# Performance work log

Measured on AMD Instinct MI355X. Metric: run time of the kernel, lower is better.

The kernel has to match this reference:

```python
import jax, jax.numpy as jnp
import numpy as np

TEXT_MAP_W, BOX_W, CONF_W = 1.0, 1.0, 1.0
LOG_CLAMP = -100.0  # torch F.binary_cross_entropy clamps log terms at -100


def _bce(p, t):
    logp = jnp.maximum(jnp.log(p), LOG_CLAMP)
    log1mp = jnp.maximum(jnp.log1p(-p), LOG_CLAMP)
    return -(t * logp + (1.0 - t) * log1mp)


def _smooth_l1(pred, tgt):
    d = jnp.abs(pred - tgt)
    return jnp.where(d < 1.0, 0.5 * d * d, d - 0.5)


def setup_inputs() -> dict:
    key = jax.random.key(0)
    ks = jax.random.split(key, 6)
    B, H, W, N = 16, 512, 512, 256
    return {
        "text_map_pred": jax.random.uniform(ks[0], (B, 1, H, W), jnp.float32),
        "text_map_tgt": jax.random.uniform(ks[1], (B, 1, H, W), jnp.float32),
        "confidence_pred": jax.random.uniform(ks[2], (B, 1, H, W), jnp.float32),
        "bbox_pred": jax.random.uniform(ks[3], (B, 4, H, W), jnp.float32),
        "box_conf": jax.random.uniform(ks[4], (B, N), jnp.float32),
        "box_xyxy": jax.random.randint(ks[5], (B, N, 4), 0, W, jnp.int64 if jax.config.read('jax_enable_x64') else jnp.int32),
        "box_mask": jnp.ones((B, N), dtype=bool),
    }


def reference(text_map_pred, text_map_tgt, confidence_pred, bbox_pred,
              box_conf, box_xyxy, box_mask):
    B, _, H, W = text_map_pred.shape
    N = box_conf.shape[1]

    # text map loss: pixelwise BCE, mean over all pixels
    text_map_loss = _bce(text_map_pred, text_map_tgt).mean()

    x1 = box_xyxy[..., 0]; y1 = box_xyxy[..., 1]
    x2 = box_xyxy[..., 2]; y2 = box_xyxy[..., 3]
    cx = (x1 + x2) // 2  # int((x1+x2)/2) for nonneg coords
    cy = (y1 + y2) // 2
    valid = box_mask & (cx >= 0) & (cx < W) & (cy >= 0) & (cy < H)  # [B,N]

    cx_c = jnp.clip(cx, 0, W - 1)
    cy_c = jnp.clip(cy, 0, H - 1)
    bi = jnp.arange(B)[:, None]  # [B,1]

    pred_box = bbox_pred[bi, :, cy_c, cx_c]          # [B,N,4]
    pred_cnf = confidence_pred[bi, 0, cy_c, cx_c]    # [B,N]

    fW = jnp.asarray(W, text_map_pred.dtype)
    fH = jnp.asarray(H, text_map_pred.dtype)
    tgt_box = jnp.stack([x1 / fW, y1 / fH, x2 / fW, y2 / fH], axis=-1)  # [B,N,4]

    box_l1 = _smooth_l1(pred_box, tgt_box).mean(axis=-1)  # per-box mean over 4 coords
    conf_l = _bce(pred_cnf, box_conf)                      # [B,N]

    vf = valid.astype(text_map_pred.dtype)
    total_boxes = vf.sum()
    denom = jnp.maximum(total_boxes, 1.0)
    any_valid = total_boxes > 0
    box_loss = jnp.where(any_valid, (box_l1 * vf).sum() / denom, 0.0)
    confidence_loss = jnp.where(any_valid, (conf_l * vf).sum() / denom, 0.0)

    total_loss = (TEXT_MAP_W * text_map_loss + BOX_W * box_loss
                  + CONF_W * confidence_loss)
    return jnp.stack([total_loss, text_map_loss, box_loss, confidence_loss])
```

## Files before the change

kernel.cpp:

```cpp
#include <hip/hip_runtime.h>

namespace {

constexpr int B = 16, H = 512, W = 512, N = 256;
constexpr int HWc = H * W;
constexpr int NBLK = 2048;
constexpr int NTHR = 256;
constexpr float LOG2_CLAMP = -144.26950408889634f;
constexpr float LN2 = 0.69314718055994531f;

constexpr int WS_L1 = NBLK, WS_CL = NBLK + 16, WS_VF = NBLK + 32;

__device__ __forceinline__ float bce2(float p, float t) {
    float m1 = fmaxf(__log2f(p), LOG2_CLAMP);
    float m2 = fmaxf(__log2f(1.0f - p), LOG2_CLAMP);
    return fmaf(t, m2 - m1, -m2);
}

__device__ __forceinline__ float smooth_l1(float pred, float tgt) {
    float d = fabsf(pred - tgt);
    return d < 1.0f ? 0.5f * d * d : d - 0.5f;
}

__device__ __forceinline__ float block_reduce_sum(float v) {
    __shared__ float smem[8];
    for (int off = 32; off > 0; off >>= 1)
        v += __shfl_down(v, off, 64);
    int lane = threadIdx.x & 63, wid = threadIdx.x >> 6;
    __syncthreads();
    if (lane == 0) smem[wid] = v;
    __syncthreads();
    if (threadIdx.x == 0) {
        float s = 0.0f;
        int nw = (int)(blockDim.x >> 6);
        for (int i = 0; i < nw; ++i) s += smem[i];
        v = s;
    }
    return v;
}

__global__ __launch_bounds__(NTHR) void main_kernel(
        const float4* __restrict__ p4,
        const float4* __restrict__ t4,
        const float*  __restrict__ conf_pred,
        const float*  __restrict__ bbox_pred,
        const float*  __restrict__ box_conf,
        const int*    __restrict__ box_xyxy,
        const int*    __restrict__ box_mask,
        float* __restrict__ ws) {
    const int n4 = B * HWc / 4;
    int idx = blockIdx.x * NTHR + threadIdx.x;
    float acc = 0.0f;
    #pragma unroll 2
    for (int i = idx; i < n4; i += NBLK * NTHR) {
        float4 p = p4[i];
        float4 t = t4[i];
        acc += bce2(p.x, t.x) + bce2(p.y, t.y) + bce2(p.z, t.z) + bce2(p.w, t.w);
    }
    float s = block_reduce_sum(acc);
    if (threadIdx.x == 0) ws[blockIdx.x] = s;

    if (blockIdx.x < B) {
        int b = blockIdx.x, n = threadIdx.x;
        int bi = b * N + n;
        int4 xy = reinterpret_cast<const int4*>(box_xyxy)[bi];
        int cx = (xy.x + xy.z) >> 1;
        int cy = (xy.y + xy.w) >> 1;
        bool valid = (box_mask[bi] != 0) && cx >= 0 && cx < W && cy >= 0 && cy < H;
        int cxc = min(max(cx, 0), W - 1);
        int cyc = min(max(cy, 0), H - 1);

        int base = ((b * 4) * H + cyc) * W + cxc;
        float l1 = 0.25f * (smooth_l1(bbox_pred[base          ], (float)xy.x * (1.0f / W)) +
                            smooth_l1(bbox_pred[base +     HWc], (float)xy.y * (1.0f / H)) +
                            smooth_l1(bbox_pred[base + 2 * HWc], (float)xy.z * (1.0f / W)) +
                            smooth_l1(bbox_pred[base + 3 * HWc], (float)xy.w * (1.0f / H)));
        float cl = bce2(conf_pred[(b * H + cyc) * W + cxc], box_conf[bi]);

        float vf = valid ? 1.0f : 0.0f;
        float s1 = block_reduce_sum(l1 * vf);
        float s2 = block_reduce_sum(cl * vf);
        float s3 = block_reduce_sum(vf);
        if (threadIdx.x == 0) {
            ws[WS_L1 + b] = s1;
            ws[WS_CL + b] = s2;
            ws[WS_VF + b] = s3;
        }
    }
}

__global__ __launch_bounds__(512) void finalize_kernel(
        const float* __restrict__ ws, float* __restrict__ out) {
    float s = 0.0f;
    #pragma unroll
    for (int i = threadIdx.x; i < NBLK; i += 512) s += ws[i];
    float text_sum = block_reduce_sum(s);

    float v1 = threadIdx.x < 16 ? ws[WS_L1 + threadIdx.x] : 0.0f;
    float v2 = threadIdx.x < 16 ? ws[WS_CL + threadIdx.x] : 0.0f;
    float v3 = threadIdx.x < 16 ? ws[WS_VF + threadIdx.x] : 0.0f;
    float s1 = block_reduce_sum(v1);
    float s2 = block_reduce_sum(v2);
    float s3 = block_reduce_sum(v3);

    if (threadIdx.x == 0) {
        float text = text_sum * (LN2 / (float)(B * HWc));
        float denom = fmaxf(s3, 1.0f);
        bool any = s3 > 0.0f;
        float box  = any ? s1 / denom : 0.0f;
        float conf = any ? (s2 * LN2) / denom : 0.0f;
        out[0] = text + box + conf;
        out[1] = text;
        out[2] = box;
        out[3] = conf;
    }
}

}

extern "C" void kernel_launch(void* const* d_in, const int* in_sizes, int n_in,
                              void* d_out, int out_size, void* d_ws, size_t ws_size,
                              hipStream_t stream) {
    const float* text_pred = (const float*)d_in[0];
    const float* text_tgt  = (const float*)d_in[1];
    const float* conf_pred = (const float*)d_in[2];
    const float* bbox_pred = (const float*)d_in[3];
    const float* box_conf  = (const float*)d_in[4];
    const int*   box_xyxy  = (const int*)d_in[5];
    const int*   box_mask  = (const int*)d_in[6];

    float* out = (float*)d_out;
    float* ws  = (float*)d_ws;

    main_kernel<<<NBLK, NTHR, 0, stream>>>(
        (const float4*)text_pred, (const float4*)text_tgt,
        conf_pred, bbox_pred, box_conf, box_xyxy, box_mask, ws);
    finalize_kernel<<<1, 512, 0, stream>>>(ws, out);
}
```

Before: 15.55 us.

## Fuse finalize into main kernel via last-block atomic reduction

Drops the separate finalize launch. Each block atomically adds its partial sums into a small set of global slots, and the last block to finish (found with an atomic counter) reduces the slots and writes the four outputs. The grid is also halved to 1024 blocks, each doing a fixed, fully unrolled 4 iterations. This removes one kernel launch and the workspace round trip, in exchange for atomic contention on 32 slots and a counter that relies on modulo wraparound across calls.

```diff
diff --git a/kernel.cpp b/kernel.cpp
--- a/kernel.cpp
+++ b/kernel.cpp
@@ -4,12 +4,16 @@
 
 constexpr int B = 16, H = 512, W = 512, N = 256;
 constexpr int HWc = H * W;
-constexpr int NBLK = 2048;
+constexpr int NBLK = 1024;
 constexpr int NTHR = 256;
+constexpr int TEXT_SLOTS = 32;
 constexpr float LOG2_CLAMP = -144.26950408889634f;
 constexpr float LN2 = 0.69314718055994531f;
 
-constexpr int WS_L1 = NBLK, WS_CL = NBLK + 16, WS_VF = NBLK + 32;
+__device__ float    g_slot[TEXT_SLOTS + 3 * 16];
+__device__ unsigned g_cnt;
+
+constexpr int SL_L1 = TEXT_SLOTS, SL_CL = TEXT_SLOTS + 16, SL_VF = TEXT_SLOTS + 32;
 
 __device__ __forceinline__ float bce2(float p, float t) {
     float m1 = fmaxf(__log2f(p), LOG2_CLAMP);
@@ -23,23 +27,18 @@
 }
 
 __device__ __forceinline__ float block_reduce_sum(float v) {
-    __shared__ float smem[8];
+    __shared__ float smem[4];
     for (int off = 32; off > 0; off >>= 1)
         v += __shfl_down(v, off, 64);
     int lane = threadIdx.x & 63, wid = threadIdx.x >> 6;
     __syncthreads();
     if (lane == 0) smem[wid] = v;
     __syncthreads();
-    if (threadIdx.x == 0) {
-        float s = 0.0f;
-        int nw = (int)(blockDim.x >> 6);
-        for (int i = 0; i < nw; ++i) s += smem[i];
-        v = s;
-    }
+    if (threadIdx.x == 0) v = smem[0] + smem[1] + smem[2] + smem[3];
     return v;
 }
 
-__global__ __launch_bounds__(NTHR) void main_kernel(
+__global__ __launch_bounds__(NTHR) void fused_kernel(
         const float4* __restrict__ p4,
         const float4* __restrict__ t4,
         const float*  __restrict__ conf_pred,
@@ -47,18 +46,19 @@
         const float*  __restrict__ box_conf,
         const int*    __restrict__ box_xyxy,
         const int*    __restrict__ box_mask,
-        float* __restrict__ ws) {
-    const int n4 = B * HWc / 4;
+        float* __restrict__ out) {
     int idx = blockIdx.x * NTHR + threadIdx.x;
     float acc = 0.0f;
-    #pragma unroll 2
-    for (int i = idx; i < n4; i += NBLK * NTHR) {
+    #pragma unroll
+    for (int it = 0; it < 4; ++it) {
+        int i = idx + it * (NBLK * NTHR);
         float4 p = p4[i];
         float4 t = t4[i];
         acc += bce2(p.x, t.x) + bce2(p.y, t.y) + bce2(p.z, t.z) + bce2(p.w, t.w);
     }
     float s = block_reduce_sum(acc);
-    if (threadIdx.x == 0) ws[blockIdx.x] = s;
+    if (threadIdx.x == 0)
+        atomicAdd(&g_slot[blockIdx.x & (TEXT_SLOTS - 1)], s);
 
     if (blockIdx.x < B) {
         int b = blockIdx.x, n = threadIdx.x;
@@ -82,37 +82,42 @@
         float s2 = block_reduce_sum(cl * vf);
         float s3 = block_reduce_sum(vf);
         if (threadIdx.x == 0) {
-            ws[WS_L1 + b] = s1;
-            ws[WS_CL + b] = s2;
-            ws[WS_VF + b] = s3;
+            atomicAdd(&g_slot[SL_L1 + b], s1);
+            atomicAdd(&g_slot[SL_CL + b], s2);
+            atomicAdd(&g_slot[SL_VF + b], s3);
         }
     }
-}
 
-__global__ __launch_bounds__(512) void finalize_kernel(
-        const float* __restrict__ ws, float* __restrict__ out) {
-    float s = 0.0f;
-    #pragma unroll
-    for (int i = threadIdx.x; i < NBLK; i += 512) s += ws[i];
-    float text_sum = block_reduce_sum(s);
+    __shared__ bool is_last;
+    if (threadIdx.x == 0) {
+        __threadfence();
+        unsigned old = atomicAdd(&g_cnt, 1u);
+        is_last = ((old & (unsigned)(NBLK - 1)) == (unsigned)(NBLK - 1));
+    }
+    __syncthreads();
 
-    float v1 = threadIdx.x < 16 ? ws[WS_L1 + threadIdx.x] : 0.0f;
-    float v2 = threadIdx.x < 16 ? ws[WS_CL + threadIdx.x] : 0.0f;
-    float v3 = threadIdx.x < 16 ? ws[WS_VF + threadIdx.x] : 0.0f;
-    float s1 = block_reduce_sum(v1);
-    float s2 = block_reduce_sum(v2);
-    float s3 = block_reduce_sum(v3);
-
-    if (threadIdx.x == 0) {
-        float text = text_sum * (LN2 / (float)(B * HWc));
-        float denom = fmaxf(s3, 1.0f);
-        bool any = s3 > 0.0f;
-        float box  = any ? s1 / denom : 0.0f;
-        float conf = any ? (s2 * LN2) / denom : 0.0f;
-        out[0] = text + box + conf;
-        out[1] = text;
-        out[2] = box;
-        out[3] = conf;
+    if (is_last) {
+        int i = threadIdx.x;
+        float v = (i < TEXT_SLOTS + 48) ? atomicExch(&g_slot[i], 0.0f) : 0.0f;
+        float vt = (i < TEXT_SLOTS) ? v : 0.0f;
+        float v1 = (i >= SL_L1 && i < SL_L1 + 16) ? v : 0.0f;
+        float v2 = (i >= SL_CL && i < SL_CL + 16) ? v : 0.0f;
+        float v3 = (i >= SL_VF && i < SL_VF + 16) ? v : 0.0f;
+        float text_sum = block_reduce_sum(vt);
+        float s1 = block_reduce_sum(v1);
+        float s2 = block_reduce_sum(v2);
+        float s3 = block_reduce_sum(v3);
+        if (threadIdx.x == 0) {
+            float text = text_sum * (LN2 / (float)(B * HWc));
+            float denom = fmaxf(s3, 1.0f);
+            bool any = s3 > 0.0f;
+            float box  = any ? s1 / denom : 0.0f;
+            float conf = any ? (s2 * LN2) / denom : 0.0f;
+            out[0] = text + box + conf;
+            out[1] = text;
+            out[2] = box;
+            out[3] = conf;
+        }
     }
 }
 
@@ -130,10 +135,8 @@
     const int*   box_mask  = (const int*)d_in[6];
 
     float* out = (float*)d_out;
-    float* ws  = (float*)d_ws;
 
-    main_kernel<<<NBLK, NTHR, 0, stream>>>(
+    fused_kernel<<<NBLK, NTHR, 0, stream>>>(
         (const float4*)text_pred, (const float4*)text_tgt,
-        conf_pred, bbox_pred, box_conf, box_xyxy, box_mask, ws);
-    finalize_kernel<<<1, 512, 0, stream>>>(ws, out);
+        conf_pred, bbox_pred, box_conf, box_xyxy, box_mask, out);
 }
```

Measured after the change: 39.32 us. 2.53x slower.
